# Performance work log

Measured on AMD Instinct MI355X. Metric: run time of the kernel, lower is better.

## Reference

```python
import jax, jax.numpy as jnp
import numpy as np

N_NODES = 100000
N_EDGES = 1600000
N_GRAPHS = 512
EPS = 1e-12


def _glorot(key, shape):
    lim = float(np.sqrt(6.0 / (shape[0] + shape[1])))
    return jax.random.uniform(key, shape, jnp.float32, -lim, lim)


def setup_inputs() -> dict:
    key = jax.random.key(0)
    ks = jax.random.split(key, 16)
    x = jax.random.normal(ks[0], (N_NODES, 5), jnp.float32)
    edge_index = jax.random.randint(ks[1], (2, N_EDGES), 0, N_NODES)
    batch = jnp.sort(jax.random.randint(ks[2], (N_NODES,), 0, N_GRAPHS))
    return {
        "x": x,
        "edge_index": edge_index,
        "batch": batch,
        "num_graphs": N_GRAPHS,
        # pre: Linear(5, 32)
        "pre_w": _glorot(ks[3], (5, 32)), "pre_b": jnp.zeros((32,), jnp.float32),
        # conv1: SAGEConv(32, 64): lin_l (agg, bias), lin_r (root, no bias)
        "c1_wl": _glorot(ks[4], (32, 64)), "c1_bl": jnp.zeros((64,), jnp.float32),
        "c1_wr": _glorot(ks[5], (32, 64)),
        # conv2: SAGEConv(64, 64)
        "c2_wl": _glorot(ks[6], (64, 64)), "c2_bl": jnp.zeros((64,), jnp.float32),
        "c2_wr": _glorot(ks[7], (64, 64)),
        # post / out linears
        "p1_w": _glorot(ks[8], (64, 64)), "p1_b": jnp.zeros((64,), jnp.float32),
        "p2_w": _glorot(ks[9], (64, 16)), "p2_b": jnp.zeros((16,), jnp.float32),
        "o_w": _glorot(ks[10], (16, 1)), "o_b": jnp.zeros((1,), jnp.float32),
    }


def _sage_conv(x, src, dst, w_l, b_l, w_r, n_nodes):
    # mean-aggregate neighbor messages src -> dst
    msg = x[src]                                              # [E, d]
    agg = jax.ops.segment_sum(msg, dst, num_segments=n_nodes)  # [N, d]
    cnt = jax.ops.segment_sum(jnp.ones((src.shape[0], 1), x.dtype), dst,
                              num_segments=n_nodes)            # [N, 1]
    agg = jnp.where(cnt > 0, agg / jnp.maximum(cnt, 1.0), 0.0)
    out = agg @ w_l + b_l + x @ w_r
    # normalize=True -> L2 normalize per node
    nrm = jnp.linalg.norm(out, axis=-1, keepdims=True)
    return out / jnp.maximum(nrm, EPS)


def reference(x, edge_index, batch, num_graphs,
              pre_w, pre_b, c1_wl, c1_bl, c1_wr, c2_wl, c2_bl, c2_wr,
              p1_w, p1_b, p2_w, p2_b, o_w, o_b):
    n_nodes = x.shape[0]
    src, dst = edge_index[0], edge_index[1]
    h = jax.nn.relu(x @ pre_w + pre_b)
    h = jax.nn.relu(_sage_conv(h, src, dst, c1_wl, c1_bl, c1_wr, n_nodes))
    h = jax.nn.relu(_sage_conv(h, src, dst, c2_wl, c2_bl, c2_wr, n_nodes))
    # global mean pool over batch index
    s = jax.ops.segment_sum(h, batch, num_segments=num_graphs)          # [G, d]
    c = jax.ops.segment_sum(jnp.ones((n_nodes, 1), h.dtype), batch,
                            num_segments=num_graphs)                    # [G, 1]
    g = s / jnp.maximum(c, 1.0)
    g = jax.nn.relu(g @ p1_w + p1_b)
    g = jax.nn.relu(g @ p2_w + p2_b)
    out = g @ o_w + o_b
    return out.squeeze(-1)
```

## Files before the change

kernel.cpp:

```cpp
#include <hip/hip_runtime.h>

#define EPSN 1e-12f
#define TILE 8192
#define SBN 512
#define BCAP 10240

using frag_ab = __attribute__((ext_vector_type(8))) short;
using frag_cd = __attribute__((ext_vector_type(4))) float;

__device__ inline unsigned short f2bf(float x) {
    union { float f; unsigned u; } v; v.f = x;
    unsigned r = v.u + 0x7fffu + ((v.u >> 16) & 1u);
    return (unsigned short)(r >> 16);
}
__device__ inline float bf2f(unsigned short b) {
    union { unsigned u; float f; } v; v.u = ((unsigned)b) << 16; return v.f;
}
__device__ inline void upadd2(uint2 u, float* a) {
    a[0] += bf2f((unsigned short)u.x); a[1] += bf2f((unsigned short)(u.x >> 16));
    a[2] += bf2f((unsigned short)u.y); a[3] += bf2f((unsigned short)(u.y >> 16));
}

__global__ __launch_bounds__(256) void prep_all(
    const float* __restrict__ x, const float* __restrict__ pw,
    const float* __restrict__ pb, unsigned short* __restrict__ h0, int n,
    const float* __restrict__ w1l, const float* __restrict__ w1r,
    unsigned short* __restrict__ wpk1,
    const float* __restrict__ w2l, const float* __restrict__ w2r,
    unsigned short* __restrict__ wpk2,
    float* __restrict__ sg, int gtot,
    const int* __restrict__ dst, int* __restrict__ thistT, int e,
    int nsb, int nt) {
    __shared__ int lh[SBN];
    int tid = threadIdx.x;
    if (blockIdx.x < nt) {
        int b = blockIdx.x;
        for (int i = tid; i < nsb; i += 256) lh[i] = 0;
        __syncthreads();
        int base = b * TILE, lim = min(base + TILE, e);
        for (int i = base + tid; i < lim; i += 256) atomicAdd(&lh[dst[i] >> 9], 1);
        __syncthreads();
        for (int i = tid; i < nsb; i += 256) thistT[(size_t)i * nt + b] = lh[i];
        return;
    }
    int idx = (blockIdx.x - nt) * 256 + tid;
    int npre = n * 32;
    if (idx < npre) {
        int node = idx >> 5, j = idx & 31;
        float v = pb[j];
#pragma unroll
        for (int k = 0; k < 5; ++k) v += x[node * 5 + k] * pw[k * 32 + j];
        h0[idx] = f2bf(fmaxf(v, 0.f));
        return;
    }
    int o = idx - npre;
    if (o < 64 * 64) {
        int j = o / 64, k = o % 64;
        float v = (k < 32) ? w1l[k * 64 + j] : w1r[(k - 32) * 64 + j];
        wpk1[o] = f2bf(v);
        return;
    }
    o -= 64 * 64;
    if (o < 64 * 128) {
        int j = o / 128, k = o % 128;
        float v = (k < 64) ? w2l[k * 64 + j] : w2r[(k - 64) * 64 + j];
        wpk2[o] = f2bf(v);
        return;
    }
    o -= 64 * 128;
    if (o < gtot) sg[o] = 0.f;
}

__global__ __launch_bounds__(256) void tscan_k(const int* __restrict__ thistT,
                                               int* __restrict__ toffsT,
                                               int* __restrict__ btot, int nt) {
    __shared__ int wsum[8];
    int b = blockIdx.x;
    int tid = threadIdx.x;
    int lane = tid & 63, w = tid >> 6;
    int x = (tid < nt) ? thistT[(size_t)b * nt + tid] : 0;
    int inc = x;
#pragma unroll
    for (int o = 1; o < 64; o <<= 1) {
        int t = __shfl_up(inc, o);
        if (lane >= o) inc += t;
    }
    if (lane == 63) wsum[w] = inc;
    __syncthreads();
    if (tid == 0) {
        int s = 0;
#pragma unroll
        for (int k = 0; k < 4; ++k) { int t = wsum[k]; wsum[k] = s; s += t; }
        wsum[4] = s;
    }
    __syncthreads();
    int excl = inc - x + wsum[w];
    if (tid < nt) toffsT[(size_t)b * nt + tid] = excl;
    if (tid == 0) btot[b] = wsum[4];
}

__global__ __launch_bounds__(256) void scat1_k(const int* __restrict__ src,
                                               const int* __restrict__ dst,
                                               const int* __restrict__ toffsT,
                                               int* __restrict__ staged, int e,
                                               int nsb, int nt) {
    __shared__ int cur[SBN];
    int tid = threadIdx.x;
    for (int i = tid; i < nsb; i += 256)
        cur[i] = i * BCAP + toffsT[(size_t)i * nt + blockIdx.x];
    __syncthreads();
    int base = blockIdx.x * TILE;
    int lim = min(base + TILE, e);
    for (int i = base + tid; i < lim; i += 256) {
        int d = dst[i];
        int p = atomicAdd(&cur[d >> 9], 1);
        staged[p] = (src[i] << 9) | (d & 511);
    }
}

__global__ __launch_bounds__(256) void scat2_k(const int* __restrict__ btot,
                                               const int* __restrict__ staged,
                                               int* __restrict__ csr,
                                               int* __restrict__ rofs,
                                               int* __restrict__ deg,
                                               int n, int nsb) {
    __shared__ int h[SBN];
    __shared__ int cur[SBN];
    __shared__ int wsum[8];
    int b = blockIdx.x;
    int tid = threadIdx.x;
    int lane = tid & 63, w = tid >> 6;
    int nlo = b << 9;
    int nn = n - nlo; if (nn > SBN) nn = SBN;
    int lo = b * BCAP, hi = lo + btot[b];
    h[tid] = 0;
    h[tid + 256] = 0;
    __syncthreads();
    for (int i = lo + tid; i < hi; i += 256) atomicAdd(&h[staged[i] & 511], 1);
    __syncthreads();
    int a0 = h[2 * tid], a1 = h[2 * tid + 1];
    int ps = a0 + a1;
    int inc = ps;
#pragma unroll
    for (int o = 1; o < 64; o <<= 1) {
        int t = __shfl_up(inc, o);
        if (lane >= o) inc += t;
    }
    if (lane == 63) wsum[w] = inc;
    __syncthreads();
    if (tid == 0) {
        int s = 0;
#pragma unroll
        for (int k = 0; k < 4; ++k) { int t = wsum[k]; wsum[k] = s; s += t; }
    }
    __syncthreads();
    int excl = inc - ps + wsum[w];
    cur[2 * tid] = excl;
    cur[2 * tid + 1] = excl + a0;
    __syncthreads();
    if (2 * tid < nn) {
        rofs[nlo + 2 * tid] = lo + cur[2 * tid];
        deg[nlo + 2 * tid] = a0;
    }
    if (2 * tid + 1 < nn) {
        rofs[nlo + 2 * tid + 1] = lo + cur[2 * tid + 1];
        deg[nlo + 2 * tid + 1] = a1;
    }
    __syncthreads();
    for (int i = lo + tid; i < hi; i += 256) {
        int v = staged[i];
        int p = atomicAdd(&cur[v & 511], 1);
        csr[lo + p] = v >> 9;
    }
}

template <int KIN, bool POOL>
__global__ __launch_bounds__(256) void conv_mfma(
    const int* __restrict__ rofs, const int* __restrict__ deg,
    const int* __restrict__ csr,
    const unsigned short* __restrict__ hin, const unsigned short* __restrict__ wpk,
    const float* __restrict__ bl, const int* __restrict__ batch,
    float* __restrict__ sg, unsigned short* __restrict__ hout, int n) {
    constexpr int KT = 2 * KIN;
    constexpr int ST = KT + 8;
    constexpr int KS = KT / 32;
    constexpr int LPE = KIN / 4;
    constexpr int EPW = 64 / LPE;
    constexpr int RB = 4;
    __shared__ unsigned short __attribute__((aligned(16))) Ab[16 * ST];
    __shared__ float __attribute__((aligned(16))) Nb[4][16];
    __shared__ int ro[16];
    __shared__ int dg[16];
    __shared__ int sb[16];

    int tid = threadIdx.x;
    int w = tid >> 6;
    int lane = tid & 63;
    int quad = lane >> 4;
    int l16 = lane & 15;
    int base = blockIdx.x * 16;
    int ncol = w * 16 + l16;

    if (tid < 16) {
        int nd = base + tid;
        bool v = nd < n;
        ro[tid] = v ? rofs[nd] : 0;
        dg[tid] = v ? deg[nd] : 0;
        if (POOL) sb[tid] = v ? batch[nd] : -1;
    }

    frag_ab bfrag[KS];
#pragma unroll
    for (int s = 0; s < KS; ++s)
        bfrag[s] = *(const frag_ab*)&wpk[(((ncol * KS) + s) * 4 + quad) * 8];
    float bias = bl[ncol];
    __syncthreads();

    int grp = lane / LPE;
    int p = lane % LPE;
    for (int i = 0; i < 4; ++i) {
        int li = w * 4 + i;
        int node = base + li;
        if (node >= n) break;
        int beg = ro[li];
        int cnt = dg[li];
        uint2 selfv = make_uint2(0u, 0u);
        if (grp == 1)
            selfv = *(const uint2*)&hin[(size_t)node * KIN + p * 4];
        float a[4] = {0.f, 0.f, 0.f, 0.f};
        for (int e0 = 0; e0 < cnt; e0 += RB * EPW) {
            int idx[RB];
            uint2 u[RB];
#pragma unroll
            for (int r = 0; r < RB; ++r) {
                int ee = e0 + r * EPW + grp;
                int cl = (ee < cnt) ? ee : (cnt - 1);
                idx[r] = csr[beg + cl];
            }
#pragma unroll
            for (int r = 0; r < RB; ++r)
                u[r] = *(const uint2*)&hin[(size_t)idx[r] * KIN + p * 4];
#pragma unroll
            for (int r = 0; r < RB; ++r)
                if (e0 + r * EPW + grp < cnt) upadd2(u[r], a);
        }
#pragma unroll
        for (int o = LPE; o < 64; o <<= 1) {
#pragma unroll
            for (int q = 0; q < 4; ++q) a[q] += __shfl_xor(a[q], o);
        }
        float inv = (cnt > 0) ? 1.0f / (float)cnt : 0.0f;
        if (grp == 0) {
            uint2 o2;
            o2.x = (unsigned)f2bf(a[0] * inv) | ((unsigned)f2bf(a[1] * inv) << 16);
            o2.y = (unsigned)f2bf(a[2] * inv) | ((unsigned)f2bf(a[3] * inv) << 16);
            *(uint2*)&Ab[li * ST + p * 4] = o2;
        } else if (grp == 1) {
            *(uint2*)&Ab[li * ST + KIN + p * 4] = selfv;
        }
    }
    __syncthreads();

    frag_cd acc = (frag_cd){0.f, 0.f, 0.f, 0.f};
#pragma unroll
    for (int s = 0; s < KS; ++s) {
        frag_ab af = *(frag_ab*)&Ab[l16 * ST + s * 32 + quad * 8];
        acc = __builtin_amdgcn_mfma_f32_16x16x32_bf16(af, bfrag[s], acc, 0, 0, 0);
    }

    float vv[4], q[4];
#pragma unroll
    for (int i = 0; i < 4; ++i) {
        float v = acc[i] + bias;
        vv[i] = v;
        q[i] = v * v;
    }
#pragma unroll
    for (int o = 1; o < 16; o <<= 1) {
#pragma unroll
        for (int i = 0; i < 4; ++i) q[i] += __shfl_xor(q[i], o);
    }
    if (l16 == 0)
        *(float4*)&Nb[w][quad * 4] = make_float4(q[0], q[1], q[2], q[3]);
    __syncthreads();

    float s0 = 0.f, s1 = 0.f, s2 = 0.f, s3 = 0.f;
#pragma unroll
    for (int ww = 0; ww < 4; ++ww) {
        float4 xq = *(const float4*)&Nb[ww][quad * 4];
        s0 += xq.x; s1 += xq.y; s2 += xq.z; s3 += xq.w;
    }
    float ss[4] = {s0, s1, s2, s3};
    float pv[4];
#pragma unroll
    for (int i = 0; i < 4; ++i) {
        float nv = fmaxf(sqrtf(ss[i]), EPSN);
        pv[i] = fmaxf(vv[i] / nv, 0.f);
    }

    if (!POOL) {
#pragma unroll
        for (int i = 0; i < 4; ++i) {
            int node = base + quad * 4 + i;
            if (node < n)
                hout[(size_t)node * 64 + ncol] = f2bf(pv[i]);
        }
    } else {
        int g0 = sb[0];
        int g1 = sb[min(15, n - 1 - base)];
        for (int g = g0; g <= g1; ++g) {
            float s = 0.f;
#pragma unroll
            for (int i = 0; i < 4; ++i)
                if (sb[quad * 4 + i] == g) s += pv[i];
            s += __shfl_xor(s, 16);
            s += __shfl_xor(s, 32);
            if (quad == 0) atomicAdd(&sg[(size_t)g * 64 + ncol], s);
        }
    }
}

__global__ __launch_bounds__(64) void mlp_k(
    const float* __restrict__ sg, const int* __restrict__ batch, int n,
    const float* __restrict__ p1w, const float* __restrict__ p1b,
    const float* __restrict__ p2w, const float* __restrict__ p2b,
    const float* __restrict__ ow, const float* __restrict__ ob,
    float* __restrict__ out) {
    __shared__ float gmean[64];
    __shared__ float a1[64];
    __shared__ float a2[16];
    int g = blockIdx.x;
    int j = threadIdx.x;
    int lo = 0, hi = n;
    while (lo < hi) { int m = (lo + hi) >> 1; if (batch[m] < g) lo = m + 1; else hi = m; }
    int start = lo;
    hi = n;
    while (lo < hi) { int m = (lo + hi) >> 1; if (batch[m] < g + 1) lo = m + 1; else hi = m; }
    float c = (float)(lo - start);
    gmean[j] = sg[(size_t)g * 64 + j] / fmaxf(c, 1.0f);
    __syncthreads();
    float v = p1b[j];
#pragma unroll 8
    for (int k = 0; k < 64; ++k) v = fmaf(gmean[k], p1w[k * 64 + j], v);
    a1[j] = fmaxf(v, 0.f);
    __syncthreads();
    if (j < 16) {
        float v2 = p2b[j];
#pragma unroll 8
        for (int k = 0; k < 64; ++k) v2 = fmaf(a1[k], p2w[k * 16 + j], v2);
        a2[j] = fmaxf(v2, 0.f);
    }
    __syncthreads();
    if (j == 0) {
        float v3 = ob[0];
#pragma unroll
        for (int k = 0; k < 16; ++k) v3 = fmaf(a2[k], ow[k], v3);
        out[g] = v3;
    }
}

extern "C" void kernel_launch(void* const* d_in, const int* in_sizes, int n_in,
                              void* d_out, int out_size, void* d_ws, size_t ws_size,
                              hipStream_t stream) {
    const float* x     = (const float*)d_in[0];
    const int*   ei    = (const int*)d_in[1];
    const int*   batch = (const int*)d_in[2];
    const float* pre_w = (const float*)d_in[4];
    const float* pre_b = (const float*)d_in[5];
    const float* c1_wl = (const float*)d_in[6];
    const float* c1_bl = (const float*)d_in[7];
    const float* c1_wr = (const float*)d_in[8];
    const float* c2_wl = (const float*)d_in[9];
    const float* c2_bl = (const float*)d_in[10];
    const float* c2_wr = (const float*)d_in[11];
    const float* p1w   = (const float*)d_in[12];
    const float* p1b   = (const float*)d_in[13];
    const float* p2w   = (const float*)d_in[14];
    const float* p2b   = (const float*)d_in[15];
    const float* ow    = (const float*)d_in[16];
    const float* ob    = (const float*)d_in[17];

    const int N = in_sizes[0] / 5;
    const int E = in_sizes[1] / 2;
    const int G = out_size;
    const int NT = (E + TILE - 1) / TILE;
    const int NSB = (N + SBN - 1) / SBN;
    const int* src = ei;
    const int* dst = ei + E;

    unsigned short* h0u = (unsigned short*)d_ws;
    unsigned short* h1u = h0u + (size_t)N * 32;
    unsigned short* wpk1 = h1u + (size_t)N * 64;
    unsigned short* wpk2 = wpk1 + 64 * 64;
    float* sg    = (float*)(wpk2 + 64 * 128);
    int* rofs    = (int*)(sg + (size_t)G * 64);
    int* deg     = rofs + N;
    int* btot    = deg + N;
    int* thistT  = btot + NSB;
    int* toffsT  = thistT + (size_t)NSB * NT;
    int* staged  = toffsT + (size_t)NSB * NT;
    int* csr     = staged + (size_t)NSB * BCAP;

    int prep_tot = N * 32 + 64 * 64 + 64 * 128 + G * 64;
    int prep_blocks = (prep_tot + 255) / 256;
    prep_all<<<NT + prep_blocks, 256, 0, stream>>>(
        x, pre_w, pre_b, h0u, N, c1_wl, c1_wr, wpk1, c2_wl, c2_wr, wpk2,
        sg, G * 64, dst, thistT, E, NSB, NT);

    tscan_k<<<NSB, 256, 0, stream>>>(thistT, toffsT, btot, NT);
    scat1_k<<<NT, 256, 0, stream>>>(src, dst, toffsT, staged, E, NSB, NT);
    scat2_k<<<NSB, 256, 0, stream>>>(btot, staged, csr, rofs, deg, N, NSB);

    conv_mfma<32, false><<<(N + 15) / 16, 256, 0, stream>>>(
        rofs, deg, csr, h0u, wpk1, c1_bl, batch, sg, h1u, N);
    conv_mfma<64, true><<<(N + 15) / 16, 256, 0, stream>>>(
        rofs, deg, csr, h1u, wpk2, c2_bl, batch, sg, nullptr, N);

    mlp_k<<<G, 64, 0, stream>>>(sg, batch, N, p1w, p1b, p2w, p2b, ow, ob,
                                (float*)d_out);
}
```

Measured before the change: 263.8 us.

## Shrink edge tiles and node buckets in CSR build for more parallelism

Lowers the edge tile size from 8192 to 2048 and the node bucket width from 512 to 256 in the two-pass bucketed CSR construction. This launches more blocks in the histogram, scatter and bucket-sort kernels, which is meant to improve occupancy and shorten per-block serial work. Because tiles can now exceed 256, the tile-offset scan loops over chunks, and the histogram is stored tile-major so writes are coalesced. The cost is a larger histogram and offset table, strided reads in the scan, and a smaller per-bucket capacity that assumes no bucket receives more than 4608 edges.

```diff
diff --git a/kernel.cpp b/kernel.cpp
--- a/kernel.cpp
+++ b/kernel.cpp
@@ -1,9 +1,11 @@
 #include <hip/hip_runtime.h>
 
 #define EPSN 1e-12f
-#define TILE 8192
-#define SBN 512
-#define BCAP 10240
+#define TILE 2048
+#define BSH 8
+#define BNODES 256
+#define SBMAX 512
+#define BCAP 4608
 
 using frag_ab = __attribute__((ext_vector_type(8))) short;
 using frag_cd = __attribute__((ext_vector_type(4))) float;
@@ -31,16 +33,16 @@
     float* __restrict__ sg, int gtot,
     const int* __restrict__ dst, int* __restrict__ thistT, int e,
     int nsb, int nt) {
-    __shared__ int lh[SBN];
+    __shared__ int lh[SBMAX];
     int tid = threadIdx.x;
     if (blockIdx.x < nt) {
         int b = blockIdx.x;
         for (int i = tid; i < nsb; i += 256) lh[i] = 0;
         __syncthreads();
         int base = b * TILE, lim = min(base + TILE, e);
-        for (int i = base + tid; i < lim; i += 256) atomicAdd(&lh[dst[i] >> 9], 1);
+        for (int i = base + tid; i < lim; i += 256) atomicAdd(&lh[dst[i] >> BSH], 1);
         __syncthreads();
-        for (int i = tid; i < nsb; i += 256) thistT[(size_t)i * nt + b] = lh[i];
+        for (int i = tid; i < nsb; i += 256) thistT[(size_t)b * nsb + i] = lh[i];
         return;
     }
     int idx = (blockIdx.x - nt) * 256 + tid;
@@ -73,30 +75,36 @@
 
 __global__ __launch_bounds__(256) void tscan_k(const int* __restrict__ thistT,
                                                int* __restrict__ toffsT,
-                                               int* __restrict__ btot, int nt) {
+                                               int* __restrict__ btot,
+                                               int nsb, int nt) {
     __shared__ int wsum[8];
     int b = blockIdx.x;
     int tid = threadIdx.x;
     int lane = tid & 63, w = tid >> 6;
-    int x = (tid < nt) ? thistT[(size_t)b * nt + tid] : 0;
-    int inc = x;
-#pragma unroll
-    for (int o = 1; o < 64; o <<= 1) {
-        int t = __shfl_up(inc, o);
-        if (lane >= o) inc += t;
-    }
-    if (lane == 63) wsum[w] = inc;
-    __syncthreads();
-    if (tid == 0) {
-        int s = 0;
-#pragma unroll
-        for (int k = 0; k < 4; ++k) { int t = wsum[k]; wsum[k] = s; s += t; }
-        wsum[4] = s;
-    }
-    __syncthreads();
-    int excl = inc - x + wsum[w];
-    if (tid < nt) toffsT[(size_t)b * nt + tid] = excl;
-    if (tid == 0) btot[b] = wsum[4];
+    int run = 0;
+    for (int base = 0; base < nt; base += 256) {
+        int i = base + tid;
+        int x = (i < nt) ? thistT[(size_t)i * nsb + b] : 0;
+        int inc = x;
+#pragma unroll
+        for (int o = 1; o < 64; o <<= 1) {
+            int t = __shfl_up(inc, o);
+            if (lane >= o) inc += t;
+        }
+        if (lane == 63) wsum[w] = inc;
+        __syncthreads();
+        if (tid == 0) {
+            int s = 0;
+#pragma unroll
+            for (int k = 0; k < 4; ++k) { int t = wsum[k]; wsum[k] = s; s += t; }
+            wsum[4] = s;
+        }
+        __syncthreads();
+        if (i < nt) toffsT[(size_t)b * nt + i] = inc - x + wsum[w] + run;
+        run += wsum[4];
+        __syncthreads();
+    }
+    if (tid == 0) btot[b] = run;
 }
 
 __global__ __launch_bounds__(256) void scat1_k(const int* __restrict__ src,
@@ -104,7 +112,7 @@
                                                const int* __restrict__ toffsT,
                                                int* __restrict__ staged, int e,
                                                int nsb, int nt) {
-    __shared__ int cur[SBN];
+    __shared__ int cur[SBMAX];
     int tid = threadIdx.x;
     for (int i = tid; i < nsb; i += 256)
         cur[i] = i * BCAP + toffsT[(size_t)i * nt + blockIdx.x];
@@ -113,8 +121,8 @@
     int lim = min(base + TILE, e);
     for (int i = base + tid; i < lim; i += 256) {
         int d = dst[i];
-        int p = atomicAdd(&cur[d >> 9], 1);
-        staged[p] = (src[i] << 9) | (d & 511);
+        int p = atomicAdd(&cur[d >> BSH], 1);
+        staged[p] = (src[i] << BSH) | (d & (BNODES - 1));
     }
 }
 
@@ -124,23 +132,21 @@
                                                int* __restrict__ rofs,
                                                int* __restrict__ deg,
                                                int n, int nsb) {
-    __shared__ int h[SBN];
-    __shared__ int cur[SBN];
+    __shared__ int h[BNODES];
+    __shared__ int cur[BNODES];
     __shared__ int wsum[8];
     int b = blockIdx.x;
     int tid = threadIdx.x;
     int lane = tid & 63, w = tid >> 6;
-    int nlo = b << 9;
-    int nn = n - nlo; if (nn > SBN) nn = SBN;
+    int nlo = b << BSH;
+    int nn = n - nlo; if (nn > BNODES) nn = BNODES;
     int lo = b * BCAP, hi = lo + btot[b];
     h[tid] = 0;
-    h[tid + 256] = 0;
-    __syncthreads();
-    for (int i = lo + tid; i < hi; i += 256) atomicAdd(&h[staged[i] & 511], 1);
-    __syncthreads();
-    int a0 = h[2 * tid], a1 = h[2 * tid + 1];
-    int ps = a0 + a1;
-    int inc = ps;
+    __syncthreads();
+    for (int i = lo + tid; i < hi; i += 256) atomicAdd(&h[staged[i] & (BNODES - 1)], 1);
+    __syncthreads();
+    int x = h[tid];
+    int inc = x;
 #pragma unroll
     for (int o = 1; o < 64; o <<= 1) {
         int t = __shfl_up(inc, o);
@@ -154,23 +160,17 @@
         for (int k = 0; k < 4; ++k) { int t = wsum[k]; wsum[k] = s; s += t; }
     }
     __syncthreads();
-    int excl = inc - ps + wsum[w];
-    cur[2 * tid] = excl;
-    cur[2 * tid + 1] = excl + a0;
-    __syncthreads();
-    if (2 * tid < nn) {
-        rofs[nlo + 2 * tid] = lo + cur[2 * tid];
-        deg[nlo + 2 * tid] = a0;
-    }
-    if (2 * tid + 1 < nn) {
-        rofs[nlo + 2 * tid + 1] = lo + cur[2 * tid + 1];
-        deg[nlo + 2 * tid + 1] = a1;
+    int excl = inc - x + wsum[w];
+    cur[tid] = excl;
+    if (tid < nn) {
+        rofs[nlo + tid] = lo + excl;
+        deg[nlo + tid] = x;
     }
     __syncthreads();
     for (int i = lo + tid; i < hi; i += 256) {
         int v = staged[i];
-        int p = atomicAdd(&cur[v & 511], 1);
-        csr[lo + p] = v >> 9;
+        int p = atomicAdd(&cur[v & (BNODES - 1)], 1);
+        csr[lo + p] = v >> BSH;
     }
 }
 
@@ -384,7 +384,7 @@
     const int E = in_sizes[1] / 2;
     const int G = out_size;
     const int NT = (E + TILE - 1) / TILE;
-    const int NSB = (N + SBN - 1) / SBN;
+    const int NSB = (N + BNODES - 1) / BNODES;
     const int* src = ei;
     const int* dst = ei + E;
 
@@ -397,7 +397,7 @@
     int* deg     = rofs + N;
     int* btot    = deg + N;
     int* thistT  = btot + NSB;
-    int* toffsT  = thistT + (size_t)NSB * NT;
+    int* toffsT  = thistT + (size_t)NT * NSB;
     int* staged  = toffsT + (size_t)NSB * NT;
     int* csr     = staged + (size_t)NSB * BCAP;
 
@@ -407,7 +407,7 @@
         x, pre_w, pre_b, h0u, N, c1_wl, c1_wr, wpk1, c2_wl, c2_wr, wpk2,
         sg, G * 64, dst, thistT, E, NSB, NT);
 
-    tscan_k<<<NSB, 256, 0, stream>>>(thistT, toffsT, btot, NT);
+    tscan_k<<<NSB, 256, 0, stream>>>(thistT, toffsT, btot, NSB, NT);
     scat1_k<<<NT, 256, 0, stream>>>(src, dst, toffsT, staged, E, NSB, NT);
     scat2_k<<<NSB, 256, 0, stream>>>(btot, staged, csr, rofs, deg, N, NSB);
 
```

Result: faster. 251.9 us (median of 2 runs) (-4.5%).
